# Kernel optimization log

Hardware: AMD Instinct MI355X
Metric: run time of the kernel (lower is better)

Reference implementation:

```python
import jax, jax.numpy as jnp
import numpy as np

B, S, D = 4, 2048, 1024
H, DK = 16, 64
DOUT = 1024

def setup_inputs() -> dict:
    key = jax.random.key(0)
    ks = jax.random.split(key, 9)
    sc_in = 1.0 / np.sqrt(D)
    sc_cat = 1.0 / np.sqrt(H * DK)
    x = jax.random.normal(ks[0], (B, S, D), dtype=jnp.float32)
    Wq = jax.random.uniform(ks[1], (H, D, DK), jnp.float32, -sc_in, sc_in)
    bq = jax.random.uniform(ks[2], (H, DK), jnp.float32, -sc_in, sc_in)
    Wk = jax.random.uniform(ks[3], (H, D, DK), jnp.float32, -sc_in, sc_in)
    bk = jax.random.uniform(ks[4], (H, DK), jnp.float32, -sc_in, sc_in)
    Wv = jax.random.uniform(ks[5], (H, D, DK), jnp.float32, -sc_in, sc_in)
    bv = jax.random.uniform(ks[6], (H, DK), jnp.float32, -sc_in, sc_in)
    Wo = jax.random.uniform(ks[7], (H * DK, DOUT), jnp.float32, -sc_cat, sc_cat)
    bo = jax.random.uniform(ks[8], (DOUT,), jnp.float32, -sc_cat, sc_cat)
    return {"x": x, "Wq": Wq, "bq": bq, "Wk": Wk, "bk": bk, "Wv": Wv, "bv": bv, "Wo": Wo, "bo": bo}

def reference(x, Wq, bq, Wk, bk, Wv, bv, Wo, bo):
    # Per-head linear projections batched over heads: [B,S,D] x [H,D,K] -> [B,H,S,K]
    Q = jnp.einsum('bsd,hdk->bhsk', x, Wq) + bq[None, :, None, :]
    K = jnp.einsum('bsd,hdk->bhsk', x, Wk) + bk[None, :, None, :]
    V = jnp.einsum('bsd,hdk->bhsk', x, Wv) + bv[None, :, None, :]
    scale = 1.0 / jnp.sqrt(jnp.asarray(DK, dtype=x.dtype))
    scores = jnp.einsum('bhsk,bhtk->bhst', Q, K) * scale  # [B,H,S,S]
    attn = jax.nn.softmax(scores, axis=-1)
    heads = jnp.einsum('bhst,bhtk->bhsk', attn, V)  # [B,H,S,K]
    # concat heads along feature dim (head order = concat order)
    cat = jnp.transpose(heads, (0, 2, 1, 3)).reshape(x.shape[0], x.shape[1], H * DK)
    return cat @ Wo + bo
```

## Files before the change

### kernel.cpp

```cpp
#include <hip/hip_runtime.h>
#include <hip/hip_bf16.h>
#include <stdint.h>

typedef unsigned short u16;
typedef __attribute__((ext_vector_type(8))) short short8;
typedef __attribute__((ext_vector_type(4))) float f32x4;
typedef __attribute__((ext_vector_type(4))) unsigned short u16x4;

#define DEV static __device__ __forceinline__


DEV u16 f2bf(float f) {
  __hip_bfloat16 b = __float2bfloat16(f);
  return *(u16*)&b;
}

DEV void stage16(const u16* g, u16* l) {
  __builtin_amdgcn_global_load_lds((const __attribute__((address_space(1))) void*)g,
                                   (__attribute__((address_space(3))) void*)l, 16, 0, 0);
}

__global__ __launch_bounds__(256) void cvt_kernel(
    const float* __restrict__ x, const float* __restrict__ Wq,
    const float* __restrict__ Wk, const float* __restrict__ Wv,
    const float* __restrict__ Wo,
    u16* __restrict__ xb, u16* __restrict__ Wt, u16* __restrict__ Wot)
{
  int idx = blockIdx.x * 256 + threadIdx.x;
  if (idx < 1048576) {
    int i = idx * 8;
    f32x4 v0 = *(const f32x4*)&x[i];
    f32x4 v1 = *(const f32x4*)&x[i + 4];
    short8 o;
    o[0]=f2bf(v0[0]); o[1]=f2bf(v0[1]); o[2]=f2bf(v0[2]); o[3]=f2bf(v0[3]);
    o[4]=f2bf(v1[0]); o[5]=f2bf(v1[1]); o[6]=f2bf(v1[2]); o[7]=f2bf(v1[3]);
    *(short8*)&xb[i] = o;
  } else if (idx < 1835008) {
    int t = (idx - 1048576) * 4;
    int w = t >> 20; int r = t & 1048575; int n = r >> 10; int d0 = r & 1023;
    const float* W = (w == 0) ? Wq : (w == 1) ? Wk : Wv;
    int h = n >> 6, k = n & 63;
    u16x4 o;
    #pragma unroll
    for (int u = 0; u < 4; u++) o[u] = f2bf(W[(size_t)(h*1024 + d0 + u)*64 + k]);
    *(u16x4*)&Wt[t] = o;
  } else if (idx < 2097152) {
    int t = (idx - 1835008) * 4;
    int n = t >> 10, d0 = t & 1023;
    u16x4 o;
    #pragma unroll
    for (int u = 0; u < 4; u++) o[u] = f2bf(Wo[(size_t)(d0 + u)*1024 + n]);
    *(u16x4*)&Wot[t] = o;
  }
}

DEV void gemm_mainloop(const u16* __restrict__ A, const u16* __restrict__ Bt,
                       int m0, int n0, u16* As, u16* Bs, f32x4 acc[4][4])
{
  const int tid = threadIdx.x;
  const int lane = tid & 63, wid = tid >> 6;
  const int wr = wid >> 1, wc = wid & 1;
  const int qr = lane & 15, g = lane >> 4;
  const int c0 = wid * 2, rA = lane >> 2, cA = (lane & 3) * 8;

  #pragma unroll
  for (int i = 0; i < 4; i++)
    #pragma unroll
    for (int j = 0; j < 4; j++) acc[i][j] = (f32x4){0.f, 0.f, 0.f, 0.f};

  for (int kt = 0; kt < 1024; kt += 32) {
    #pragma unroll
    for (int q = 0; q < 2; q++) {
      const int c = c0 + q;
      stage16(A  + (size_t)(m0 + c*16 + rA)*1024 + kt + cA, &As[c*512]);
      stage16(Bt + (size_t)(n0 + c*16 + rA)*1024 + kt + cA, &Bs[c*512]);
    }
    __syncthreads();
    short8 af[4], bfr[4];
    #pragma unroll
    for (int i = 0; i < 4; i++) af[i]  = *(const short8*)&As[(wr*64 + i*16 + qr)*32 + g*8];
    #pragma unroll
    for (int j = 0; j < 4; j++) bfr[j] = *(const short8*)&Bs[(wc*64 + j*16 + qr)*32 + g*8];
    #pragma unroll
    for (int i = 0; i < 4; i++)
      #pragma unroll
      for (int j = 0; j < 4; j++)
        acc[i][j] = __builtin_amdgcn_mfma_f32_16x16x32_bf16(af[i], bfr[j], acc[i][j], 0, 0, 0);
    __syncthreads();
  }
}

__global__ __launch_bounds__(256) void qkv_gemm_kernel(
    const u16* __restrict__ A, const u16* __restrict__ WtAll,
    const float* __restrict__ bq, const float* __restrict__ bk, const float* __restrict__ bv,
    u16* __restrict__ Qo, u16* __restrict__ Ko, u16* __restrict__ Vo)
{
  __shared__ __align__(128) u16 As[4096];
  __shared__ __align__(128) u16 Bs[4096];
  const int lane = threadIdx.x & 63, wid = threadIdx.x >> 6;
  const int wr = wid >> 1, wc = wid & 1;
  const int qr = lane & 15, g = lane >> 4;
  const int m0 = blockIdx.y * 128, n0 = blockIdx.x * 128;
  const int mode = blockIdx.z;
  const u16* Bt = WtAll + (size_t)mode * 1048576;
  const float* bias = (mode == 0) ? bq : (mode == 1) ? bk : bv;
  const float osc = (mode == 0) ? 0.1803368867f : 1.0f;

  f32x4 acc[4][4];
  gemm_mainloop(A, Bt, m0, n0, As, Bs, acc);

  if (mode == 2) {
    #pragma unroll
    for (int i = 0; i < 4; i++) {
      const int mrow = m0 + wr*64 + i*16 + g*4;
      const int b = mrow >> 11, s = mrow & 2047;
      #pragma unroll
      for (int j = 0; j < 4; j++) {
        const int n = n0 + wc*64 + j*16 + qr;
        const float bz = bias[n];
        u16x4 v;
        #pragma unroll
        for (int r = 0; r < 4; r++) v[r] = f2bf(acc[i][j][r] + bz);
        *(u16x4*)&Vo[((size_t)(b*16 + (n >> 6))*64 + (n & 63))*2048 + s] = v;
      }
    }
  } else {
    u16* O = (mode == 0) ? Qo : Ko;
    #pragma unroll
    for (int i = 0; i < 4; i++) {
      const int mrow = m0 + wr*64 + i*16 + g*4;
      const int b = mrow >> 11, s = mrow & 2047;
      #pragma unroll
      for (int j = 0; j < 4; j++) {
        const int n = n0 + wc*64 + j*16 + qr;
        const float bz = bias[n];
        const size_t base = ((size_t)(b*16 + (n >> 6))*2048 + s)*64 + (n & 63);
        #pragma unroll
        for (int r = 0; r < 4; r++) O[base + (size_t)r*64] = f2bf((acc[i][j][r] + bz) * osc);
      }
    }
  }
}

__global__ __launch_bounds__(256, 4) void attn_kernel(
    const u16* __restrict__ Q, const u16* __restrict__ K,
    const u16* __restrict__ Vt, u16* __restrict__ cat)
{
  __shared__ __align__(16) u16 Ks[2][2048];
  __shared__ __align__(16) u16 Vs[2][2048];
  __shared__ __align__(16) u16 Pl[5120];
  const int lane = threadIdx.x & 63, w = threadIdx.x >> 6;
  const int bid = blockIdx.x;
  const int logical = (bid & 7) * 128 + (bid >> 3);
  const int bh = logical >> 4;
  const int xq = logical & 15;
  const int b = bh >> 4, h = bh & 15;
  const int q0 = xq * 128 + w * 32;
  const int qr = lane & 15, g = lane >> 4;
  u16* P0 = &Pl[(w*2 + 0)*640];
  u16* P1 = &Pl[(w*2 + 1)*640];

  const u16* Qb = Q  + (size_t)bh * 131072;
  const u16* Kb = K  + (size_t)bh * 131072;
  const u16* Vb = Vt + (size_t)bh * 131072;

  const int krow = 8*w + (lane >> 3), kc_ = lane & 7;
  const size_t ksrc = (size_t)krow*64 + (size_t)((kc_ ^ (lane >> 3)) * 8);
  const int vrow = 16*w + (lane >> 2), vc_ = lane & 3;
  const size_t vsrc = (size_t)vrow*2048 + (size_t)((vc_ ^ ((lane >> 2) & 3)) * 8);

  const int kro0 = qr*64        + ((g     ^ (qr & 7)) * 8);
  const int kro1 = qr*64        + (((4+g) ^ (qr & 7)) * 8);
  const int kro2 = (16+qr)*64   + ((g     ^ (qr & 7)) * 8);
  const int kro3 = (16+qr)*64   + (((4+g) ^ (qr & 7)) * 8);
  const int vro  = qr*32        + ((g ^ (qr & 3)) * 8);

  const short8 qa0 = *(const short8*)&Qb[(size_t)(q0 + qr)*64 + g*8];
  const short8 qb0 = *(const short8*)&Qb[(size_t)(q0 + qr)*64 + 32 + g*8];
  const short8 qa1 = *(const short8*)&Qb[(size_t)(q0 + 16 + qr)*64 + g*8];
  const short8 qb1 = *(const short8*)&Qb[(size_t)(q0 + 16 + qr)*64 + 32 + g*8];

  const short ONE = (short)0x3F80;
  const short8 ones = {ONE, ONE, ONE, ONE, ONE, ONE, ONE, ONE};

  f32x4 o0[4], o1[4];
  #pragma unroll
  for (int d = 0; d < 4; d++) { o0[d] = (f32x4){0.f,0.f,0.f,0.f}; o1[d] = (f32x4){0.f,0.f,0.f,0.f}; }
  f32x4 ol0 = {0.f,0.f,0.f,0.f}, ol1 = {0.f,0.f,0.f,0.f};

  stage16(Kb + ksrc, &Ks[0][w*512]);
  stage16(Vb + vsrc, &Vs[0][w*512]);
  __syncthreads();

  for (int tt = 0; tt < 2048; tt += 32) {
    const int cur = (tt >> 5) & 1, nxt = cur ^ 1;
    const int tn = (tt + 32) & 2047;
    stage16(Kb + (size_t)tn*64 + ksrc, &Ks[nxt][w*512]);
    stage16(Vb + vsrc + tn,            &Vs[nxt][w*512]);

    const u16* Kc = Ks[cur];
    short8 kc0 = *(const short8*)&Kc[kro0];
    short8 kc1 = *(const short8*)&Kc[kro1];
    short8 kc2 = *(const short8*)&Kc[kro2];
    short8 kc3 = *(const short8*)&Kc[kro3];

    f32x4 s00 = {0.f,0.f,0.f,0.f}, s01 = {0.f,0.f,0.f,0.f};
    f32x4 s10 = {0.f,0.f,0.f,0.f}, s11 = {0.f,0.f,0.f,0.f};
    s00 = __builtin_amdgcn_mfma_f32_16x16x32_bf16(kc0, qa0, s00, 0, 0, 0);
    s00 = __builtin_amdgcn_mfma_f32_16x16x32_bf16(kc1, qb0, s00, 0, 0, 0);
    s01 = __builtin_amdgcn_mfma_f32_16x16x32_bf16(kc2, qa0, s01, 0, 0, 0);
    s01 = __builtin_amdgcn_mfma_f32_16x16x32_bf16(kc3, qb0, s01, 0, 0, 0);
    s10 = __builtin_amdgcn_mfma_f32_16x16x32_bf16(kc0, qa1, s10, 0, 0, 0);
    s10 = __builtin_amdgcn_mfma_f32_16x16x32_bf16(kc1, qb1, s10, 0, 0, 0);
    s11 = __builtin_amdgcn_mfma_f32_16x16x32_bf16(kc2, qa1, s11, 0, 0, 0);
    s11 = __builtin_amdgcn_mfma_f32_16x16x32_bf16(kc3, qb1, s11, 0, 0, 0);

    u16x4 lo0, hi0, lo1, hi1;
    #pragma unroll
    for (int r = 0; r < 4; r++) {
      lo0[r] = f2bf(__builtin_amdgcn_exp2f(s00[r]));
      hi0[r] = f2bf(__builtin_amdgcn_exp2f(s01[r]));
      lo1[r] = f2bf(__builtin_amdgcn_exp2f(s10[r]));
      hi1[r] = f2bf(__builtin_amdgcn_exp2f(s11[r]));
    }
    *(u16x4*)&P0[qr*40 + g*4]      = lo0;
    *(u16x4*)&P0[qr*40 + 16 + g*4] = hi0;
    *(u16x4*)&P1[qr*40 + g*4]      = lo1;
    *(u16x4*)&P1[qr*40 + 16 + g*4] = hi1;
    short8 bp0 = *(const short8*)&P0[qr*40 + g*8];
    short8 bp1 = *(const short8*)&P1[qr*40 + g*8];

    ol0 = __builtin_amdgcn_mfma_f32_16x16x32_bf16(ones, bp0, ol0, 0, 0, 0);
    ol1 = __builtin_amdgcn_mfma_f32_16x16x32_bf16(ones, bp1, ol1, 0, 0, 0);

    const u16* Vc = Vs[cur];
    #pragma unroll
    for (int d = 0; d < 4; d++) {
      short8 av = *(const short8*)&Vc[d*512 + vro];
      o0[d] = __builtin_amdgcn_mfma_f32_16x16x32_bf16(av, bp0, o0[d], 0, 0, 0);
      o1[d] = __builtin_amdgcn_mfma_f32_16x16x32_bf16(av, bp1, o1[d], 0, 0, 0);
    }
    __syncthreads();
  }
  const float inv0 = 1.0f / ol0[0], inv1 = 1.0f / ol1[0];
  const size_t base0 = ((size_t)(b*2048 + q0 + qr))*1024 + h*64;
  const size_t base1 = ((size_t)(b*2048 + q0 + 16 + qr))*1024 + h*64;
  #pragma unroll
  for (int d = 0; d < 4; d++) {
    u16x4 v0, v1;
    #pragma unroll
    for (int r = 0; r < 4; r++) { v0[r] = f2bf(o0[d][r] * inv0); v1[r] = f2bf(o1[d][r] * inv1); }
    *(u16x4*)&cat[base0 + d*16 + g*4] = v0;
    *(u16x4*)&cat[base1 + d*16 + g*4] = v1;
  }
}

__global__ __launch_bounds__(256) void out_gemm_kernel(
    const u16* __restrict__ A, const u16* __restrict__ Bt,
    const float* __restrict__ bias, float* __restrict__ out)
{
  __shared__ __align__(128) u16 As[4096];
  __shared__ __align__(128) u16 Bs[4096];
  const int lane = threadIdx.x & 63, wid = threadIdx.x >> 6;
  const int wr = wid >> 1, wc = wid & 1;
  const int qr = lane & 15, g = lane >> 4;
  const int m0 = blockIdx.y * 128, n0 = blockIdx.x * 128;

  f32x4 acc[4][4];
  gemm_mainloop(A, Bt, m0, n0, As, Bs, acc);

  #pragma unroll
  for (int i = 0; i < 4; i++) {
    const int mrow = m0 + wr*64 + i*16 + g*4;
    #pragma unroll
    for (int j = 0; j < 4; j++) {
      const int n = n0 + wc*64 + j*16 + qr;
      const float bz = bias[n];
      #pragma unroll
      for (int r = 0; r < 4; r++) out[(size_t)(mrow + r)*1024 + n] = acc[i][j][r] + bz;
    }
  }
}

extern "C" void kernel_launch(void* const* d_in, const int* in_sizes, int n_in,
                              void* d_out, int out_size, void* d_ws, size_t ws_size,
                              hipStream_t stream) {
  const float* x  = (const float*)d_in[0];
  const float* Wq = (const float*)d_in[1];
  const float* bq = (const float*)d_in[2];
  const float* Wk = (const float*)d_in[3];
  const float* bk = (const float*)d_in[4];
  const float* Wv = (const float*)d_in[5];
  const float* bv = (const float*)d_in[6];
  const float* Wo = (const float*)d_in[7];
  const float* bo = (const float*)d_in[8];
  float* out = (float*)d_out;
  char* ws = (char*)d_ws;

  u16* xb  = (u16*)(ws);
  u16* Wt  = (u16*)(ws + 16777216);
  u16* Wot = (u16*)(ws + 23068672);
  u16* Qb  = (u16*)(ws + 25165824);
  u16* Kb  = (u16*)(ws + 41943040);
  u16* Vt  = (u16*)(ws + 58720256);
  u16* cat = xb;

  cvt_kernel<<<8192, 256, 0, stream>>>(x, Wq, Wk, Wv, Wo, xb, Wt, Wot);
  qkv_gemm_kernel<<<dim3(8, 64, 3), 256, 0, stream>>>(xb, Wt, bq, bk, bv, Qb, Kb, Vt);
  attn_kernel<<<1024, 256, 0, stream>>>(Qb, Kb, Vt, cat);
  out_gemm_kernel<<<dim3(8, 64), 256, 0, stream>>>(cat, Wot, bo, out);
}
```

Measured before the change: 219.2 us.

## Enlarge attention query tile to 512 per block with 8 waves

The attention kernel now runs 512-thread blocks in which each wave handles 64 query rows instead of 32. Each staged K/V tile is therefore reused across four times as many queries, which cuts global and LDS traffic per unit of work. Staging is split so four waves load K and four load V, and the V swizzle is adjusted to match. In exchange the grid shrinks to 256 blocks, so there are fewer waves per CU and more accumulator registers per wave, which may reduce latency hiding.

```diff
diff --git a/kernel.cpp b/kernel.cpp
--- a/kernel.cpp
+++ b/kernel.cpp
@@ -142,20 +142,20 @@
   }
 }
 
-__global__ __launch_bounds__(256, 4) void attn_kernel(
+__global__ __launch_bounds__(512, 2) void attn_kernel(
     const u16* __restrict__ Q, const u16* __restrict__ K,
     const u16* __restrict__ Vt, u16* __restrict__ cat)
 {
   __shared__ __align__(16) u16 Ks[2][2048];
   __shared__ __align__(16) u16 Vs[2][2048];
-  __shared__ __align__(16) u16 Pl[5120];
+  __shared__ __align__(16) u16 Pl[10240];
   const int lane = threadIdx.x & 63, w = threadIdx.x >> 6;
   const int bid = blockIdx.x;
-  const int logical = (bid & 7) * 128 + (bid >> 3);
-  const int bh = logical >> 4;
-  const int xq = logical & 15;
+  const int logical = (bid & 7) * 32 + (bid >> 3);
+  const int bh = logical >> 2;
+  const int xq = logical & 3;
   const int b = bh >> 4, h = bh & 15;
-  const int q0 = xq * 128 + w * 32;
+  const int q0 = xq * 512 + w * 64;
   const int qr = lane & 15, g = lane >> 4;
   u16* P0 = &Pl[(w*2 + 0)*640];
   u16* P1 = &Pl[(w*2 + 1)*640];
@@ -164,94 +164,93 @@
   const u16* Kb = K  + (size_t)bh * 131072;
   const u16* Vb = Vt + (size_t)bh * 131072;
 
-  const int krow = 8*w + (lane >> 3), kc_ = lane & 7;
-  const size_t ksrc = (size_t)krow*64 + (size_t)((kc_ ^ (lane >> 3)) * 8);
-  const int vrow = 16*w + (lane >> 2), vc_ = lane & 3;
-  const size_t vsrc = (size_t)vrow*2048 + (size_t)((vc_ ^ ((lane >> 2) & 3)) * 8);
+  const int isK = (w < 4);
+  const int krow = 8*w + (lane >> 3);
+  const size_t ksrc = (size_t)krow*64 + (size_t)(((lane & 7) ^ (lane >> 3)) * 8);
+  const int vw = w - 4, vrow = 16*vw + (lane >> 2);
+  const size_t vsrc = (size_t)vrow*2048 + (size_t)(((lane & 3) ^ ((lane >> 3) & 3)) * 8);
+  u16* kdst0 = &Ks[0][w*512];       u16* kdst1 = &Ks[1][w*512];
+  u16* vdst0 = &Vs[0][vw*512];      u16* vdst1 = &Vs[1][vw*512];
 
   const int kro0 = qr*64        + ((g     ^ (qr & 7)) * 8);
   const int kro1 = qr*64        + (((4+g) ^ (qr & 7)) * 8);
   const int kro2 = (16+qr)*64   + ((g     ^ (qr & 7)) * 8);
   const int kro3 = (16+qr)*64   + (((4+g) ^ (qr & 7)) * 8);
-  const int vro  = qr*32        + ((g ^ (qr & 3)) * 8);
-
-  const short8 qa0 = *(const short8*)&Qb[(size_t)(q0 + qr)*64 + g*8];
-  const short8 qb0 = *(const short8*)&Qb[(size_t)(q0 + qr)*64 + 32 + g*8];
-  const short8 qa1 = *(const short8*)&Qb[(size_t)(q0 + 16 + qr)*64 + g*8];
-  const short8 qb1 = *(const short8*)&Qb[(size_t)(q0 + 16 + qr)*64 + 32 + g*8];
+  const int vro  = qr*32        + ((g ^ ((qr >> 1) & 3)) * 8);
+
+  short8 qa[4], qb_[4];
+  #pragma unroll
+  for (int qs = 0; qs < 4; qs++) {
+    qa[qs]  = *(const short8*)&Qb[(size_t)(q0 + qs*16 + qr)*64 + g*8];
+    qb_[qs] = *(const short8*)&Qb[(size_t)(q0 + qs*16 + qr)*64 + 32 + g*8];
+  }
 
   const short ONE = (short)0x3F80;
   const short8 ones = {ONE, ONE, ONE, ONE, ONE, ONE, ONE, ONE};
 
-  f32x4 o0[4], o1[4];
-  #pragma unroll
-  for (int d = 0; d < 4; d++) { o0[d] = (f32x4){0.f,0.f,0.f,0.f}; o1[d] = (f32x4){0.f,0.f,0.f,0.f}; }
-  f32x4 ol0 = {0.f,0.f,0.f,0.f}, ol1 = {0.f,0.f,0.f,0.f};
-
-  stage16(Kb + ksrc, &Ks[0][w*512]);
-  stage16(Vb + vsrc, &Vs[0][w*512]);
+  f32x4 o[4][4];
+  #pragma unroll
+  for (int qs = 0; qs < 4; qs++)
+    #pragma unroll
+    for (int d = 0; d < 4; d++) o[qs][d] = (f32x4){0.f,0.f,0.f,0.f};
+  f32x4 ol[4] = {{0.f,0.f,0.f,0.f},{0.f,0.f,0.f,0.f},{0.f,0.f,0.f,0.f},{0.f,0.f,0.f,0.f}};
+
+  if (isK) stage16(Kb + ksrc, kdst0); else stage16(Vb + vsrc, vdst0);
   __syncthreads();
 
   for (int tt = 0; tt < 2048; tt += 32) {
-    const int cur = (tt >> 5) & 1, nxt = cur ^ 1;
+    const int cur = (tt >> 5) & 1;
     const int tn = (tt + 32) & 2047;
-    stage16(Kb + (size_t)tn*64 + ksrc, &Ks[nxt][w*512]);
-    stage16(Vb + vsrc + tn,            &Vs[nxt][w*512]);
+    if (isK) stage16(Kb + (size_t)tn*64 + ksrc, cur ? kdst0 : kdst1);
+    else     stage16(Vb + vsrc + tn,            cur ? vdst0 : vdst1);
 
     const u16* Kc = Ks[cur];
+    const u16* Vc = Vs[cur];
     short8 kc0 = *(const short8*)&Kc[kro0];
     short8 kc1 = *(const short8*)&Kc[kro1];
     short8 kc2 = *(const short8*)&Kc[kro2];
     short8 kc3 = *(const short8*)&Kc[kro3];
-
-    f32x4 s00 = {0.f,0.f,0.f,0.f}, s01 = {0.f,0.f,0.f,0.f};
-    f32x4 s10 = {0.f,0.f,0.f,0.f}, s11 = {0.f,0.f,0.f,0.f};
-    s00 = __builtin_amdgcn_mfma_f32_16x16x32_bf16(kc0, qa0, s00, 0, 0, 0);
-    s00 = __builtin_amdgcn_mfma_f32_16x16x32_bf16(kc1, qb0, s00, 0, 0, 0);
-    s01 = __builtin_amdgcn_mfma_f32_16x16x32_bf16(kc2, qa0, s01, 0, 0, 0);
-    s01 = __builtin_amdgcn_mfma_f32_16x16x32_bf16(kc3, qb0, s01, 0, 0, 0);
-    s10 = __builtin_amdgcn_mfma_f32_16x16x32_bf16(kc0, qa1, s10, 0, 0, 0);
-    s10 = __builtin_amdgcn_mfma_f32_16x16x32_bf16(kc1, qb1, s10, 0, 0, 0);
-    s11 = __builtin_amdgcn_mfma_f32_16x16x32_bf16(kc2, qa1, s11, 0, 0, 0);
-    s11 = __builtin_amdgcn_mfma_f32_16x16x32_bf16(kc3, qb1, s11, 0, 0, 0);
-
-    u16x4 lo0, hi0, lo1, hi1;
-    #pragma unroll
-    for (int r = 0; r < 4; r++) {
-      lo0[r] = f2bf(__builtin_amdgcn_exp2f(s00[r]));
-      hi0[r] = f2bf(__builtin_amdgcn_exp2f(s01[r]));
-      lo1[r] = f2bf(__builtin_amdgcn_exp2f(s10[r]));
-      hi1[r] = f2bf(__builtin_amdgcn_exp2f(s11[r]));
-    }
-    *(u16x4*)&P0[qr*40 + g*4]      = lo0;
-    *(u16x4*)&P0[qr*40 + 16 + g*4] = hi0;
-    *(u16x4*)&P1[qr*40 + g*4]      = lo1;
-    *(u16x4*)&P1[qr*40 + 16 + g*4] = hi1;
-    short8 bp0 = *(const short8*)&P0[qr*40 + g*8];
-    short8 bp1 = *(const short8*)&P1[qr*40 + g*8];
-
-    ol0 = __builtin_amdgcn_mfma_f32_16x16x32_bf16(ones, bp0, ol0, 0, 0, 0);
-    ol1 = __builtin_amdgcn_mfma_f32_16x16x32_bf16(ones, bp1, ol1, 0, 0, 0);
-
-    const u16* Vc = Vs[cur];
+    short8 vv0 = *(const short8*)&Vc[0*512 + vro];
+    short8 vv1 = *(const short8*)&Vc[1*512 + vro];
+    short8 vv2 = *(const short8*)&Vc[2*512 + vro];
+    short8 vv3 = *(const short8*)&Vc[3*512 + vro];
+
+    #pragma unroll
+    for (int qs = 0; qs < 4; qs++) {
+      f32x4 sl = {0.f,0.f,0.f,0.f}, sh = {0.f,0.f,0.f,0.f};
+      sl = __builtin_amdgcn_mfma_f32_16x16x32_bf16(kc0, qa[qs],  sl, 0, 0, 0);
+      sl = __builtin_amdgcn_mfma_f32_16x16x32_bf16(kc1, qb_[qs], sl, 0, 0, 0);
+      sh = __builtin_amdgcn_mfma_f32_16x16x32_bf16(kc2, qa[qs],  sh, 0, 0, 0);
+      sh = __builtin_amdgcn_mfma_f32_16x16x32_bf16(kc3, qb_[qs], sh, 0, 0, 0);
+      u16x4 lo, hi;
+      #pragma unroll
+      for (int r = 0; r < 4; r++) {
+        lo[r] = f2bf(__builtin_amdgcn_exp2f(sl[r]));
+        hi[r] = f2bf(__builtin_amdgcn_exp2f(sh[r]));
+      }
+      u16* P = (qs & 1) ? P1 : P0;
+      *(u16x4*)&P[qr*40 + g*4]      = lo;
+      *(u16x4*)&P[qr*40 + 16 + g*4] = hi;
+      short8 bp = *(const short8*)&P[qr*40 + g*8];
+      ol[qs] = __builtin_amdgcn_mfma_f32_16x16x32_bf16(ones, bp, ol[qs], 0, 0, 0);
+      o[qs][0] = __builtin_amdgcn_mfma_f32_16x16x32_bf16(vv0, bp, o[qs][0], 0, 0, 0);
+      o[qs][1] = __builtin_amdgcn_mfma_f32_16x16x32_bf16(vv1, bp, o[qs][1], 0, 0, 0);
+      o[qs][2] = __builtin_amdgcn_mfma_f32_16x16x32_bf16(vv2, bp, o[qs][2], 0, 0, 0);
+      o[qs][3] = __builtin_amdgcn_mfma_f32_16x16x32_bf16(vv3, bp, o[qs][3], 0, 0, 0);
+    }
+    __syncthreads();
+  }
+  #pragma unroll
+  for (int qs = 0; qs < 4; qs++) {
+    const float inv = 1.0f / ol[qs][0];
+    const size_t base = ((size_t)(b*2048 + q0 + qs*16 + qr))*1024 + h*64;
     #pragma unroll
     for (int d = 0; d < 4; d++) {
-      short8 av = *(const short8*)&Vc[d*512 + vro];
-      o0[d] = __builtin_amdgcn_mfma_f32_16x16x32_bf16(av, bp0, o0[d], 0, 0, 0);
-      o1[d] = __builtin_amdgcn_mfma_f32_16x16x32_bf16(av, bp1, o1[d], 0, 0, 0);
-    }
-    __syncthreads();
-  }
-  const float inv0 = 1.0f / ol0[0], inv1 = 1.0f / ol1[0];
-  const size_t base0 = ((size_t)(b*2048 + q0 + qr))*1024 + h*64;
-  const size_t base1 = ((size_t)(b*2048 + q0 + 16 + qr))*1024 + h*64;
-  #pragma unroll
-  for (int d = 0; d < 4; d++) {
-    u16x4 v0, v1;
-    #pragma unroll
-    for (int r = 0; r < 4; r++) { v0[r] = f2bf(o0[d][r] * inv0); v1[r] = f2bf(o1[d][r] * inv1); }
-    *(u16x4*)&cat[base0 + d*16 + g*4] = v0;
-    *(u16x4*)&cat[base1 + d*16 + g*4] = v1;
+      u16x4 v;
+      #pragma unroll
+      for (int r = 0; r < 4; r++) v[r] = f2bf(o[qs][d][r] * inv);
+      *(u16x4*)&cat[base + d*16 + g*4] = v;
+    }
   }
 }
 
@@ -307,6 +306,6 @@
 
   cvt_kernel<<<8192, 256, 0, stream>>>(x, Wq, Wk, Wv, Wo, xb, Wt, Wot);
   qkv_gemm_kernel<<<dim3(8, 64, 3), 256, 0, stream>>>(xb, Wt, bq, bk, bv, Qb, Kb, Vt);
-  attn_kernel<<<1024, 256, 0, stream>>>(Qb, Kb, Vt, cat);
+  attn_kernel<<<256, 512, 0, stream>>>(Qb, Kb, Vt, cat);
   out_gemm_kernel<<<dim3(8, 64), 256, 0, stream>>>(cat, Wot, bo, out);
 }
```

Result: faster. 202.1 us (-7.8%).
